# Kernel tuning notes

Hardware: AMD Instinct MI355X
Metric: run time of the kernel (lower is better)

Reference implementation:

```python
import jax, jax.numpy as jnp
import numpy as np

N_HEADS = 16
D_HEAD = 64
D_MODEL = 1024


def apply_rotary_emb(t, cos, sin):
    # t: (B, H, T, D), cos/sin: (T, D//2) -> half-split rotation
    d2 = t.shape[-1] // 2
    t1, t2 = t[..., :d2], t[..., d2:]
    cos = cos[None, None, :, :]
    sin = sin[None, None, :, :]
    return jnp.concatenate([t1 * cos - t2 * sin, t1 * sin + t2 * cos], axis=-1)


def setup_inputs() -> dict:
    key = jax.random.key(0)
    ks = jax.random.split(key, 8)
    B, T = 2, 2048
    x = jax.random.normal(ks[0], (B, T, D_MODEL), dtype=jnp.float32)
    # rotary cache built from standard inv-freq schedule
    inv_freq = 1.0 / (10000.0 ** (jnp.arange(0, D_HEAD, 2, dtype=jnp.float32) / D_HEAD))
    ang = jnp.arange(T, dtype=jnp.float32)[:, None] * inv_freq[None, :]  # (T, D/2)
    cos, sin = jnp.cos(ang), jnp.sin(ang)
    s = 1.0 / np.sqrt(D_MODEL)
    W_q = jax.random.normal(ks[1], (D_MODEL, N_HEADS * D_HEAD), dtype=jnp.float32) * s
    W_k = jax.random.normal(ks[2], (D_MODEL, N_HEADS * D_HEAD), dtype=jnp.float32) * s
    W_v = jax.random.normal(ks[3], (D_MODEL, N_HEADS * D_HEAD), dtype=jnp.float32) * s
    W_out = jax.random.normal(ks[4], (N_HEADS * D_HEAD, D_MODEL), dtype=jnp.float32) * s
    return {"x": x, "cos": cos, "sin": sin, "W_q": W_q, "W_k": W_k, "W_v": W_v, "W_out": W_out}


def reference(x, cos, sin, W_q, W_k, W_v, W_out):
    B, T, _ = x.shape
    def split_heads(t):
        return t.reshape(B, T, N_HEADS, D_HEAD).transpose(0, 2, 1, 3)  # (B,H,T,D)
    q = split_heads(x @ W_q)
    k = split_heads(x @ W_k)
    v = split_heads(x @ W_v)
    q = apply_rotary_emb(q, cos, sin)
    k = apply_rotary_emb(k, cos, sin)
    scores = jnp.einsum('bhqd,bhkd->bhqk', q, k) / np.sqrt(D_HEAD).astype(np.float32)
    causal = jnp.triu(jnp.ones((T, T), dtype=bool), k=1)
    scores = jnp.where(causal[None, None], -jnp.inf, scores)
    attn = jax.nn.softmax(scores, axis=-1)
    z = jnp.einsum('bhqk,bhkd->bhqd', attn, v)
    z = z.transpose(0, 2, 1, 3).reshape(B, T, N_HEADS * D_HEAD)
    return z @ W_out
```

## Files before the change

### kernel.cpp

```cpp
#include <hip/hip_runtime.h>

typedef __attribute__((ext_vector_type(4))) float f32x4;
typedef __attribute__((ext_vector_type(8))) short short8;
typedef __attribute__((ext_vector_type(8))) unsigned short u16x8;
typedef __attribute__((ext_vector_type(4))) unsigned short u16x4;
typedef __attribute__((ext_vector_type(2))) unsigned int u32x2;

#define D_MODEL 1024
#define NHEADS 16
#define T_SEQ 2048
#define M_TOT 4096

__device__ __forceinline__ unsigned short f2bf(float f) {
    union { float f; unsigned int u; } v; v.f = f;
    return (unsigned short)((v.u + 0x7fffu + ((v.u >> 16) & 1u)) >> 16);
}
__device__ __forceinline__ float bf2f(unsigned short b) {
    union { unsigned int u; float f; } v; v.u = ((unsigned int)b) << 16;
    return v.f;
}
__device__ __forceinline__ unsigned int cvtpk_bf16(float lo, float hi) {
    unsigned int r;
    asm("v_cvt_pk_bf16_f32 %0, %1, %2" : "=v"(r) : "v"(lo), "v"(hi));
    return r;
}

#define GLD0(dst, addr) \
    asm volatile("global_load_dwordx4 %0, %1, off" : "=v"(dst) : "v"(addr) : "memory")
#define WAITV0() do { asm volatile("s_waitcnt vmcnt(0)" ::: "memory"); \
                      __builtin_amdgcn_sched_barrier(0); } while (0)
#define LBAR() do { asm volatile("s_waitcnt lgkmcnt(0)" ::: "memory"); \
                    __builtin_amdgcn_s_barrier(); \
                    __builtin_amdgcn_sched_barrier(0); } while (0)

__global__ __launch_bounds__(256) void convert_x_kernel(const float* __restrict__ X,
                                                        unsigned short* __restrict__ Xb) {
    const int i = (blockIdx.x * 256 + threadIdx.x) * 4;
    const float4 v = *(const float4*)(X + i);
    u16x4 r;
    r.x = f2bf(v.x); r.y = f2bf(v.y); r.z = f2bf(v.z); r.w = f2bf(v.w);
    *(u16x4*)(Xb + i) = r;
}

__global__ __launch_bounds__(256) void transpose_w_kernel(const float* __restrict__ W0,
                                                          const float* __restrict__ W1,
                                                          const float* __restrict__ W2,
                                                          const float* __restrict__ W3,
                                                          unsigned short* __restrict__ Wt0) {
    __shared__ float tile[64][65];
    const int z = blockIdx.z;
    const float* W = (z == 0) ? W0 : (z == 1) ? W1 : (z == 2) ? W2 : W3;
    unsigned short* Wt = Wt0 + (size_t)z * D_MODEL * D_MODEL;
    const int n0 = blockIdx.x * 64, k0 = blockIdx.y * 64;
    for (int i = threadIdx.x; i < 4096; i += 256) {
        const int r = i >> 6, c = i & 63;
        tile[r][c] = W[(size_t)(k0 + r) * D_MODEL + n0 + c];
    }
    __syncthreads();
    for (int i = threadIdx.x; i < 4096; i += 256) {
        const int r = i >> 6, c = i & 63;
        Wt[(size_t)(n0 + r) * D_MODEL + k0 + c] = f2bf(tile[c][r]);
    }
}

#define TN_G 128
#define BK_G 32
#define BKP_G 36

template<int MI, int OUTMODE>
__global__ __launch_bounds__(256) void gemm_kernel(
    const unsigned short* __restrict__ A,
    const unsigned short* __restrict__ Bt0,
    void* __restrict__ Cout0,
    const float* __restrict__ cosp,
    const float* __restrict__ sinp)
{
    constexpr int TMc = MI * 32;
    constexpr int NA = (TMc * 4) / 256;
    __shared__ unsigned short sA[TMc * BKP_G];
    __shared__ unsigned short sB[TN_G * BKP_G];

    const int tid = threadIdx.x;
    const int wid = tid >> 6;
    const int lane = tid & 63;
    const int quad = lane >> 4;
    const int l16 = lane & 15;
    const int wm = wid >> 1, wn = wid & 1;
    const int m0 = blockIdx.x * TMc, n0 = blockIdx.y * TN_G;
    const int z = blockIdx.z;
    const unsigned short* Bt = Bt0 + (size_t)z * D_MODEL * D_MODEL;

    f32x4 acc[MI][4] = {};

    for (int k0 = 0; k0 < D_MODEL; k0 += BK_G) {
        u16x8 av[NA], bv[2];
        #pragma unroll
        for (int i = 0; i < NA; ++i) {
            const int c = tid + i * 256, r = c >> 2, sg = (c & 3) * 8;
            av[i] = *(const u16x8*)(A + (size_t)(m0 + r) * D_MODEL + k0 + sg);
        }
        #pragma unroll
        for (int i = 0; i < 2; ++i) {
            const int c = tid + i * 256, r = c >> 2, sg = (c & 3) * 8;
            bv[i] = *(const u16x8*)(Bt + (size_t)(n0 + r) * D_MODEL + k0 + sg);
        }
        __syncthreads();
        #pragma unroll
        for (int i = 0; i < NA; ++i) {
            const int c = tid + i * 256, r = c >> 2, sg = (c & 3) * 8;
            *(u16x8*)&sA[r * BKP_G + sg] = av[i];
        }
        #pragma unroll
        for (int i = 0; i < 2; ++i) {
            const int c = tid + i * 256, r = c >> 2, sg = (c & 3) * 8;
            *(u16x8*)&sB[r * BKP_G + sg] = bv[i];
        }
        __syncthreads();

        short8 af[MI], bf[4];
        #pragma unroll
        for (int i = 0; i < MI; ++i)
            af[i] = *(const short8*)&sA[(wm * (MI * 16) + i * 16 + l16) * BKP_G + quad * 8];
        #pragma unroll
        for (int i = 0; i < 4; ++i)
            bf[i] = *(const short8*)&sB[(wn * 64 + i * 16 + l16) * BKP_G + quad * 8];
        #pragma unroll
        for (int mi = 0; mi < MI; ++mi)
            #pragma unroll
            for (int ni = 0; ni < 4; ++ni)
                acc[mi][ni] = __builtin_amdgcn_mfma_f32_16x16x32_bf16(af[mi], bf[ni], acc[mi][ni], 0, 0, 0);
    }

    if constexpr (OUTMODE == 0) {
        float* C = (float*)Cout0;
        #pragma unroll
        for (int mi = 0; mi < MI; ++mi) {
            const int mb = m0 + wm * (MI * 16) + mi * 16 + quad * 4;
            #pragma unroll
            for (int ni = 0; ni < 4; ++ni) {
                const int n = n0 + wn * 64 + ni * 16 + l16;
                #pragma unroll
                for (int r = 0; r < 4; ++r)
                    C[(size_t)(mb + r) * D_MODEL + n] = acc[mi][ni][r];
            }
        }
    } else {
        unsigned short* O = (unsigned short*)Cout0 + (size_t)z * M_TOT * D_MODEL;
        const int h = (n0 + wn * 64) >> 6;
        if (z == 2) {
            #pragma unroll
            for (int mi = 0; mi < MI; ++mi) {
                const int mb = m0 + wm * (MI * 16) + mi * 16 + quad * 4;
                const int b = mb >> 11, t = mb & (T_SEQ - 1);
                #pragma unroll
                for (int ni = 0; ni < 4; ++ni) {
                    const int d = ni * 16 + l16;
                    u16x4 pk;
                    #pragma unroll
                    for (int r = 0; r < 4; ++r) pk[r] = f2bf(acc[mi][ni][r]);
                    *(u16x4*)(O + ((size_t)(b * NHEADS + h) * 64 + d) * T_SEQ + t) = pk;
                }
            }
        } else {
            const float qs = (z == 0) ? 0.125f : 1.0f;
            #pragma unroll
            for (int mi = 0; mi < MI; ++mi) {
                #pragma unroll
                for (int r = 0; r < 4; ++r) {
                    const int m = m0 + wm * (MI * 16) + mi * 16 + quad * 4 + r;
                    const int b = m >> 11, t = m & (T_SEQ - 1);
                    const size_t rowoff = ((size_t)(b * NHEADS + h) * T_SEQ + t) * 64;
                    #pragma unroll
                    for (int ni = 0; ni < 2; ++ni) {
                        const int d = ni * 16 + l16;
                        const float c = cosp[t * 32 + d], s = sinp[t * 32 + d];
                        const float x1 = acc[mi][ni][r], x2 = acc[mi][ni + 2][r];
                        O[rowoff + d]      = f2bf((x1 * c - x2 * s) * qs);
                        O[rowoff + d + 32] = f2bf((x1 * s + x2 * c) * qs);
                    }
                }
            }
        }
    }
}

__global__ __launch_bounds__(256) void kmax_kernel(const unsigned short* __restrict__ Kg,
                                                   float* __restrict__ Kseg) {
    __shared__ float red[4];
    const int seg = blockIdx.x, bh = blockIdx.y;
    const unsigned short* Kp = Kg + ((size_t)bh * T_SEQ + seg * 256) * 64;
    const int row = threadIdx.x;
    const u16x8* rp = (const u16x8*)(Kp + (size_t)row * 64);
    float s = 0.f;
    #pragma unroll
    for (int c = 0; c < 8; ++c) {
        const u16x8 v = rp[c];
        #pragma unroll
        for (int e = 0; e < 8; ++e) { const float f = bf2f(v[e]); s += f * f; }
    }
    #pragma unroll
    for (int off = 32; off >= 1; off >>= 1) s = fmaxf(s, __shfl_xor(s, off));
    if ((threadIdx.x & 63) == 0) red[threadIdx.x >> 6] = s;
    __syncthreads();
    if (threadIdx.x == 0)
        Kseg[bh * 8 + seg] = __builtin_sqrtf(fmaxf(fmaxf(red[0], red[1]), fmaxf(red[2], red[3])));
}

#define LOG2E 1.44269504f

struct AttnSmem {
    union {
        unsigned short kv[2][4][4096];
        float comb[4][64][34];
    } u;
    unsigned short P[8][16 * 64];
};

__global__ __launch_bounds__(512, 2) void attn_kernel(
    const unsigned short* __restrict__ Q,
    const unsigned short* __restrict__ Kg,
    const unsigned short* __restrict__ Vt,
    const float* __restrict__ Kseg,
    unsigned short* __restrict__ Z)
{
    __shared__ AttnSmem sm;

    const int tid = threadIdx.x;
    const int wid = tid >> 6;
    const int w4 = wid & 3;
    const int half = wid >> 2;
    const int lane = tid & 63;
    const int quad = lane >> 4;
    const int l16 = lane & 15;
    const int srow = tid >> 3;
    const int sslot = tid & 7;
    const int wslot = sslot ^ (srow & 7);
    const int sxK = (quad ^ (l16 & 7)) << 3;
    const int ph8 = (l16 & 7) << 3;

    const int flat = blockIdx.x + 16 * blockIdx.y;
    const int xcd = flat & 7, idx = flat >> 3;
    const int bh = xcd * 4 + (idx & 3);
    const int x = idx >> 2;

    const int qA = x, qB = 31 - x;
    const int jend = 31 - x;

    const unsigned short* Qp = Q + (size_t)bh * T_SEQ * 64;
    const unsigned short* Kp = Kg + (size_t)bh * T_SEQ * 64;
    const unsigned short* Vp = Vt + (size_t)bh * 64 * T_SEQ;

    short8 aqA[2], aqB[2];
    {
        const unsigned short* qr = Qp + (size_t)(qA * 64 + w4 * 16 + l16) * 64 + quad * 8;
        aqA[0] = *(const short8*)(qr);
        aqA[1] = *(const short8*)(qr + 32);
        qr = Qp + (size_t)(qB * 64 + w4 * 16 + l16) * 64 + quad * 8;
        aqB[0] = *(const short8*)(qr);
        aqB[1] = *(const short8*)(qr + 32);
    }

    float kmx = 0.f;
    #pragma unroll
    for (int i = 0; i < 8; ++i) kmx = fmaxf(kmx, Kseg[bh * 8 + i]);

    float mQA, mQB;
    {
        float nqA = 0.f, nqB = 0.f;
        #pragma unroll
        for (int i = 0; i < 2; ++i)
            #pragma unroll
            for (int e = 0; e < 8; ++e) {
                const float fa = bf2f((unsigned short)aqA[i][e]);
                const float fb = bf2f((unsigned short)aqB[i][e]);
                nqA += fa * fa; nqB += fb * fb;
            }
        nqA += __shfl_xor(nqA, 16); nqA += __shfl_xor(nqA, 32);
        nqB += __shfl_xor(nqB, 16); nqB += __shfl_xor(nqB, 32);
        mQA = __builtin_sqrtf(nqA) * kmx * LOG2E;
        mQB = __builtin_sqrtf(nqB) * kmx * LOG2E;
    }

    auto tile_pack = [&](f32x4 (&s)[4], float mQ, float& lsum, bool msk,
                         unsigned short* Pw) {
        if (msk) {
            #pragma unroll
            for (int nt = 0; nt < 4; ++nt)
                #pragma unroll
                for (int r = 0; r < 4; ++r)
                    if (nt * 16 + quad * 4 + r > w4 * 16 + l16) s[nt][r] = -1e30f;
        }
        #pragma unroll
        for (int nt = 0; nt < 4; ++nt) {
            const float p0 = __builtin_exp2f(s[nt][0] * LOG2E - mQ);
            const float p1 = __builtin_exp2f(s[nt][1] * LOG2E - mQ);
            const float p2 = __builtin_exp2f(s[nt][2] * LOG2E - mQ);
            const float p3 = __builtin_exp2f(s[nt][3] * LOG2E - mQ);
            lsum += (p0 + p1) + (p2 + p3);
            const unsigned int w0 = cvtpk_bf16(p0, p1);
            const unsigned int w1 = cvtpk_bf16(p2, p3);
            *(u32x2*)&Pw[l16 * 64 + ((nt * 16 + quad * 4) ^ ph8)] = (u32x2){w0, w1};
        }
    };

    f32x4 oA[4] = {}, oB[4] = {};
    float lA = 0.f, lB = 0.f;
    unsigned short* Pw = &sm.P[wid][0];

    short8 stg[4];
    auto ISSUE = [&](int t) {
        const int j0 = 2 * t, j1 = j0 + 1;
        GLD0(stg[0], Kp + (size_t)j0 * 4096 + tid * 8);
        GLD0(stg[1], Vp + (size_t)srow * 2048 + j0 * 64 + sslot * 8);
        GLD0(stg[2], Kp + (size_t)j1 * 4096 + tid * 8);
        GLD0(stg[3], Vp + (size_t)srow * 2048 + j1 * 64 + sslot * 8);
    };
    auto WRITE = [&](int b) {
        const int dst = srow * 64 + (wslot << 3);
        *(short8*)&sm.u.kv[b][0][dst] = stg[0];
        *(short8*)&sm.u.kv[b][1][dst] = stg[1];
        *(short8*)&sm.u.kv[b][2][dst] = stg[2];
        *(short8*)&sm.u.kv[b][3][dst] = stg[3];
    };

    auto COMPUTE = [&](int j, int b) {
        if (j > jend) return;
        const bool doA = (j <= x);
        const unsigned short* sKb = &sm.u.kv[b][half * 2][0];
        const unsigned short* sVb = &sm.u.kv[b][half * 2 + 1][0];
        f32x4 sA[4] = {}, sB[4] = {};
        __builtin_amdgcn_s_setprio(1);
        #pragma unroll
        for (int nt = 0; nt < 4; ++nt) {
            const int rb = (nt * 16 + l16) * 64;
            const short8 k0 = *(const short8*)&sKb[rb + sxK];
            const short8 k1 = *(const short8*)&sKb[rb + (sxK ^ 32)];
            if (doA) {
                sA[nt] = __builtin_amdgcn_mfma_f32_16x16x32_bf16(k0, aqA[0], sA[nt], 0, 0, 0);
                sA[nt] = __builtin_amdgcn_mfma_f32_16x16x32_bf16(k1, aqA[1], sA[nt], 0, 0, 0);
            }
            sB[nt] = __builtin_amdgcn_mfma_f32_16x16x32_bf16(k0, aqB[0], sB[nt], 0, 0, 0);
            sB[nt] = __builtin_amdgcn_mfma_f32_16x16x32_bf16(k1, aqB[1], sB[nt], 0, 0, 0);
        }
        __builtin_amdgcn_s_setprio(0);
        short8 pfA0 = {}, pfA1 = {};
        if (doA) {
            tile_pack(sA, mQA, lA, j == x, Pw);
            asm volatile("s_waitcnt lgkmcnt(0)" ::: "memory");
            pfA0 = *(const short8*)&Pw[l16 * 64 + ((quad * 8) ^ ph8)];
            pfA1 = *(const short8*)&Pw[l16 * 64 + ((32 + quad * 8) ^ ph8)];
        }
        tile_pack(sB, mQB, lB, j == jend, Pw);
        asm volatile("s_waitcnt lgkmcnt(0)" ::: "memory");
        const short8 pfB0 = *(const short8*)&Pw[l16 * 64 + ((quad * 8) ^ ph8)];
        const short8 pfB1 = *(const short8*)&Pw[l16 * 64 + ((32 + quad * 8) ^ ph8)];
        __builtin_amdgcn_s_setprio(1);
        #pragma unroll
        for (int dt = 0; dt < 4; ++dt) {
            const int rb = (dt * 16 + l16) * 64;
            const short8 v0 = *(const short8*)&sVb[rb + sxK];
            const short8 v1 = *(const short8*)&sVb[rb + (sxK ^ 32)];
            if (doA) {
                oA[dt] = __builtin_amdgcn_mfma_f32_16x16x32_bf16(pfA0, v0, oA[dt], 0, 0, 0);
                oA[dt] = __builtin_amdgcn_mfma_f32_16x16x32_bf16(pfA1, v1, oA[dt], 0, 0, 0);
            }
            oB[dt] = __builtin_amdgcn_mfma_f32_16x16x32_bf16(pfB0, v0, oB[dt], 0, 0, 0);
            oB[dt] = __builtin_amdgcn_mfma_f32_16x16x32_bf16(pfB1, v1, oB[dt], 0, 0, 0);
        }
        __builtin_amdgcn_s_setprio(0);
    };

    const int nr = (jend >> 1) + 1;
    ISSUE(0);
    WAITV0();
    WRITE(0);
    LBAR();
    for (int t = 0; t < nr; ++t) {
        const bool more = (t + 1 < nr);
        if (more) ISSUE(t + 1);
        COMPUTE(2 * t + half, t & 1);
        if (more) {
            WAITV0();
            WRITE((t + 1) & 1);
        }
        LBAR();
    }

    lA += __shfl_xor(lA, 16); lA += __shfl_xor(lA, 32);
    lB += __shfl_xor(lB, 16); lB += __shfl_xor(lB, 32);

    __syncthreads();
    if (half) {
        float* cb = &sm.u.comb[w4][lane][0];
        #pragma unroll
        for (int dt = 0; dt < 4; ++dt)
            #pragma unroll
            for (int r = 0; r < 4; ++r) {
                cb[dt * 4 + r]      = oA[dt][r];
                cb[16 + dt * 4 + r] = oB[dt][r];
            }
        cb[32] = lA; cb[33] = lB;
    }
    __syncthreads();
    if (half) return;

    {
        const float* cb = &sm.u.comb[w4][lane][0];
        #pragma unroll
        for (int dt = 0; dt < 4; ++dt)
            #pragma unroll
            for (int r = 0; r < 4; ++r) {
                oA[dt][r] += cb[dt * 4 + r];
                oB[dt][r] += cb[16 + dt * 4 + r];
            }
        lA += cb[32]; lB += cb[33];
    }

    const float iA = 1.f / lA, iB = 1.f / lB;
    float irA[4], irB[4];
    #pragma unroll
    for (int r = 0; r < 4; ++r) {
        const int src = (lane & 48) | (quad * 4 + r);
        irA[r] = __shfl(iA, src);
        irB[r] = __shfl(iB, src);
    }

    const int h = bh & 15, b = bh >> 4;
    #pragma unroll
    for (int dt = 0; dt < 4; ++dt)
        #pragma unroll
        for (int r = 0; r < 4; ++r) {
            const int rowA = qA * 64 + w4 * 16 + quad * 4 + r;
            const int rowB = qB * 64 + w4 * 16 + quad * 4 + r;
            const int col = h * 64 + dt * 16 + l16;
            Z[((size_t)b * T_SEQ + rowA) * D_MODEL + col] = f2bf(oA[dt][r] * irA[r]);
            Z[((size_t)b * T_SEQ + rowB) * D_MODEL + col] = f2bf(oB[dt][r] * irB[r]);
        }
}

extern "C" void kernel_launch(void* const* d_in, const int* in_sizes, int n_in,
                              void* d_out, int out_size, void* d_ws, size_t ws_size,
                              hipStream_t stream) {
    const float* x    = (const float*)d_in[0];
    const float* cosp = (const float*)d_in[1];
    const float* sinp = (const float*)d_in[2];
    const float* Wq   = (const float*)d_in[3];
    const float* Wk   = (const float*)d_in[4];
    const float* Wv   = (const float*)d_in[5];
    const float* Wo   = (const float*)d_in[6];

    char* w = (char*)d_ws;
    unsigned short* xb  = (unsigned short*)w; w += (size_t)M_TOT * D_MODEL * 2;
    unsigned short* wt  = (unsigned short*)w; w += (size_t)4 * D_MODEL * D_MODEL * 2;
    unsigned short* Qb  = (unsigned short*)w; w += (size_t)M_TOT * D_MODEL * 2;
    unsigned short* Kb  = (unsigned short*)w; w += (size_t)M_TOT * D_MODEL * 2;
    unsigned short* Vtb = (unsigned short*)w; w += (size_t)M_TOT * D_MODEL * 2;
    unsigned short* Zb  = (unsigned short*)w; w += (size_t)M_TOT * D_MODEL * 2;
    float*          Ks  = (float*)w;          w += 32 * 8 * sizeof(float);

    convert_x_kernel<<<(M_TOT * D_MODEL) / 1024, 256, 0, stream>>>(x, xb);
    transpose_w_kernel<<<dim3(16, 16, 4), 256, 0, stream>>>(Wq, Wk, Wv, Wo, wt);

    gemm_kernel<4, 1><<<dim3(M_TOT / 128, D_MODEL / 128, 3), 256, 0, stream>>>(
        xb, wt, (void*)Qb, cosp, sinp);

    kmax_kernel<<<dim3(8, 32), 256, 0, stream>>>(Kb, Ks);

    attn_kernel<<<dim3(16, 32), 512, 0, stream>>>(Qb, Kb, Vtb, Ks, Zb);

    gemm_kernel<2, 0><<<dim3(M_TOT / 64, D_MODEL / 128, 1), 256, 0, stream>>>(
        Zb, wt + (size_t)3 * D_MODEL * D_MODEL, d_out, nullptr, nullptr);
}
```

Measured before the change: 216.1 us.

## Fuse prep kernels, fold K-norm max into projection GEMM, use direct-to-LDS loads

Merges the x conversion and weight transpose into one launch. Computes per-64-row K norm maxima in the QKV GEMM epilogue, which removes the separate kmax pass that re-read K. The GEMM mainloop now uses global_load_lds to move tiles straight into unpadded shared memory, dropping the register staging and one barrier per k-step. Without padding, LDS fragment reads may see more bank conflicts, and there is still no double buffering.

```diff
diff --git a/kernel.cpp b/kernel.cpp
--- a/kernel.cpp
+++ b/kernel.cpp
@@ -33,22 +33,28 @@
                     __builtin_amdgcn_s_barrier(); \
                     __builtin_amdgcn_sched_barrier(0); } while (0)
 
-__global__ __launch_bounds__(256) void convert_x_kernel(const float* __restrict__ X,
-                                                        unsigned short* __restrict__ Xb) {
-    const int i = (blockIdx.x * 256 + threadIdx.x) * 4;
-    const float4 v = *(const float4*)(X + i);
-    u16x4 r;
-    r.x = f2bf(v.x); r.y = f2bf(v.y); r.z = f2bf(v.z); r.w = f2bf(v.w);
-    *(u16x4*)(Xb + i) = r;
-}
-
-__global__ __launch_bounds__(256) void transpose_w_kernel(const float* __restrict__ W0,
-                                                          const float* __restrict__ W1,
-                                                          const float* __restrict__ W2,
-                                                          const float* __restrict__ W3,
-                                                          unsigned short* __restrict__ Wt0) {
+#define GLDS16(gp, lp) \
+    __builtin_amdgcn_global_load_lds((const __attribute__((address_space(1))) void*)(gp), \
+                                     (__attribute__((address_space(3))) void*)(lp), 16, 0, 0)
+
+__global__ __launch_bounds__(256) void prep_kernel(const float* __restrict__ X,
+                                                   unsigned short* __restrict__ Xb,
+                                                   const float* __restrict__ W0,
+                                                   const float* __restrict__ W1,
+                                                   const float* __restrict__ W2,
+                                                   const float* __restrict__ W3,
+                                                   unsigned short* __restrict__ Wt0) {
     __shared__ float tile[64][65];
     const int z = blockIdx.z;
+    if (z >= 4) {
+        const int blk = (z - 4) * 256 + blockIdx.y * 16 + blockIdx.x;
+        const int i = (blk * 256 + threadIdx.x) * 4;
+        const float4 v = *(const float4*)(X + i);
+        u16x4 r;
+        r.x = f2bf(v.x); r.y = f2bf(v.y); r.z = f2bf(v.z); r.w = f2bf(v.w);
+        *(u16x4*)(Xb + i) = r;
+        return;
+    }
     const float* W = (z == 0) ? W0 : (z == 1) ? W1 : (z == 2) ? W2 : W3;
     unsigned short* Wt = Wt0 + (size_t)z * D_MODEL * D_MODEL;
     const int n0 = blockIdx.x * 64, k0 = blockIdx.y * 64;
@@ -65,7 +71,6 @@
 
 #define TN_G 128
 #define BK_G 32
-#define BKP_G 36
 
 template<int MI, int OUTMODE>
 __global__ __launch_bounds__(256) void gemm_kernel(
@@ -73,12 +78,13 @@
     const unsigned short* __restrict__ Bt0,
     void* __restrict__ Cout0,
     const float* __restrict__ cosp,
-    const float* __restrict__ sinp)
+    const float* __restrict__ sinp,
+    float* __restrict__ Kmax)
 {
     constexpr int TMc = MI * 32;
-    constexpr int NA = (TMc * 4) / 256;
-    __shared__ unsigned short sA[TMc * BKP_G];
-    __shared__ unsigned short sB[TN_G * BKP_G];
+    constexpr int NCHA = TMc / 16;
+    __shared__ unsigned short sA[TMc * 32];
+    __shared__ unsigned short sB[TN_G * 32];
 
     const int tid = threadIdx.x;
     const int wid = tid >> 6;
@@ -89,46 +95,37 @@
     const int m0 = blockIdx.x * TMc, n0 = blockIdx.y * TN_G;
     const int z = blockIdx.z;
     const unsigned short* Bt = Bt0 + (size_t)z * D_MODEL * D_MODEL;
+    const int srowL = lane >> 2;
+    const int scolL = (lane & 3) * 8;
 
     f32x4 acc[MI][4] = {};
 
     for (int k0 = 0; k0 < D_MODEL; k0 += BK_G) {
-        u16x8 av[NA], bv[2];
-        #pragma unroll
-        for (int i = 0; i < NA; ++i) {
-            const int c = tid + i * 256, r = c >> 2, sg = (c & 3) * 8;
-            av[i] = *(const u16x8*)(A + (size_t)(m0 + r) * D_MODEL + k0 + sg);
-        }
-        #pragma unroll
-        for (int i = 0; i < 2; ++i) {
-            const int c = tid + i * 256, r = c >> 2, sg = (c & 3) * 8;
-            bv[i] = *(const u16x8*)(Bt + (size_t)(n0 + r) * D_MODEL + k0 + sg);
+        #pragma unroll
+        for (int ch = wid; ch < NCHA + 8; ch += 4) {
+            if (ch < NCHA) {
+                GLDS16(A + (size_t)(m0 + ch * 16 + srowL) * D_MODEL + k0 + scolL,
+                       &sA[ch * 512]);
+            } else {
+                GLDS16(Bt + (size_t)(n0 + (ch - NCHA) * 16 + srowL) * D_MODEL + k0 + scolL,
+                       &sB[(ch - NCHA) * 512]);
+            }
         }
         __syncthreads();
-        #pragma unroll
-        for (int i = 0; i < NA; ++i) {
-            const int c = tid + i * 256, r = c >> 2, sg = (c & 3) * 8;
-            *(u16x8*)&sA[r * BKP_G + sg] = av[i];
-        }
-        #pragma unroll
-        for (int i = 0; i < 2; ++i) {
-            const int c = tid + i * 256, r = c >> 2, sg = (c & 3) * 8;
-            *(u16x8*)&sB[r * BKP_G + sg] = bv[i];
-        }
-        __syncthreads();
 
         short8 af[MI], bf[4];
         #pragma unroll
         for (int i = 0; i < MI; ++i)
-            af[i] = *(const short8*)&sA[(wm * (MI * 16) + i * 16 + l16) * BKP_G + quad * 8];
+            af[i] = *(const short8*)&sA[(wm * (MI * 16) + i * 16 + l16) * 32 + quad * 8];
         #pragma unroll
         for (int i = 0; i < 4; ++i)
-            bf[i] = *(const short8*)&sB[(wn * 64 + i * 16 + l16) * BKP_G + quad * 8];
+            bf[i] = *(const short8*)&sB[(wn * 64 + i * 16 + l16) * 32 + quad * 8];
         #pragma unroll
         for (int mi = 0; mi < MI; ++mi)
             #pragma unroll
             for (int ni = 0; ni < 4; ++ni)
                 acc[mi][ni] = __builtin_amdgcn_mfma_f32_16x16x32_bf16(af[mi], bf[ni], acc[mi][ni], 0, 0, 0);
+        __syncthreads();
     }
 
     if constexpr (OUTMODE == 0) {
@@ -162,6 +159,27 @@
                 }
             }
         } else {
+            if (z == 1) {
+                float mx = 0.f;
+                #pragma unroll
+                for (int mi = 0; mi < MI; ++mi)
+                    #pragma unroll
+                    for (int r = 0; r < 4; ++r) {
+                        float s = 0.f;
+                        #pragma unroll
+                        for (int ni = 0; ni < 4; ++ni) s += acc[mi][ni][r] * acc[mi][ni][r];
+                        s += __shfl_xor(s, 1); s += __shfl_xor(s, 2);
+                        s += __shfl_xor(s, 4); s += __shfl_xor(s, 8);
+                        mx = fmaxf(mx, s);
+                    }
+                mx = fmaxf(mx, __shfl_xor(mx, 16));
+                mx = fmaxf(mx, __shfl_xor(mx, 32));
+                if (lane == 0) {
+                    const int b = m0 >> 11;
+                    const int slot = ((m0 >> 7) & 15) * 2 + wm;
+                    Kmax[(size_t)(b * NHEADS + h) * 32 + slot] = __builtin_sqrtf(mx);
+                }
+            }
             const float qs = (z == 0) ? 0.125f : 1.0f;
             #pragma unroll
             for (int mi = 0; mi < MI; ++mi) {
@@ -184,28 +202,6 @@
     }
 }
 
-__global__ __launch_bounds__(256) void kmax_kernel(const unsigned short* __restrict__ Kg,
-                                                   float* __restrict__ Kseg) {
-    __shared__ float red[4];
-    const int seg = blockIdx.x, bh = blockIdx.y;
-    const unsigned short* Kp = Kg + ((size_t)bh * T_SEQ + seg * 256) * 64;
-    const int row = threadIdx.x;
-    const u16x8* rp = (const u16x8*)(Kp + (size_t)row * 64);
-    float s = 0.f;
-    #pragma unroll
-    for (int c = 0; c < 8; ++c) {
-        const u16x8 v = rp[c];
-        #pragma unroll
-        for (int e = 0; e < 8; ++e) { const float f = bf2f(v[e]); s += f * f; }
-    }
-    #pragma unroll
-    for (int off = 32; off >= 1; off >>= 1) s = fmaxf(s, __shfl_xor(s, off));
-    if ((threadIdx.x & 63) == 0) red[threadIdx.x >> 6] = s;
-    __syncthreads();
-    if (threadIdx.x == 0)
-        Kseg[bh * 8 + seg] = __builtin_sqrtf(fmaxf(fmaxf(red[0], red[1]), fmaxf(red[2], red[3])));
-}
-
 #define LOG2E 1.44269504f
 
 struct AttnSmem {
@@ -262,7 +258,7 @@
 
     float kmx = 0.f;
     #pragma unroll
-    for (int i = 0; i < 8; ++i) kmx = fmaxf(kmx, Kseg[bh * 8 + i]);
+    for (int i = 0; i < 32; ++i) kmx = fmaxf(kmx, Kseg[bh * 32 + i]);
 
     float mQA, mQB;
     {
@@ -456,18 +452,15 @@
     unsigned short* Kb  = (unsigned short*)w; w += (size_t)M_TOT * D_MODEL * 2;
     unsigned short* Vtb = (unsigned short*)w; w += (size_t)M_TOT * D_MODEL * 2;
     unsigned short* Zb  = (unsigned short*)w; w += (size_t)M_TOT * D_MODEL * 2;
-    float*          Ks  = (float*)w;          w += 32 * 8 * sizeof(float);
-
-    convert_x_kernel<<<(M_TOT * D_MODEL) / 1024, 256, 0, stream>>>(x, xb);
-    transpose_w_kernel<<<dim3(16, 16, 4), 256, 0, stream>>>(Wq, Wk, Wv, Wo, wt);
+    float*          Ks  = (float*)w;          w += 32 * 32 * sizeof(float);
+
+    prep_kernel<<<dim3(16, 16, 20), 256, 0, stream>>>(x, xb, Wq, Wk, Wv, Wo, wt);
 
     gemm_kernel<4, 1><<<dim3(M_TOT / 128, D_MODEL / 128, 3), 256, 0, stream>>>(
-        xb, wt, (void*)Qb, cosp, sinp);
-
-    kmax_kernel<<<dim3(8, 32), 256, 0, stream>>>(Kb, Ks);
+        xb, wt, (void*)Qb, cosp, sinp, Ks);
 
     attn_kernel<<<dim3(16, 32), 512, 0, stream>>>(Qb, Kb, Vtb, Ks, Zb);
 
     gemm_kernel<2, 0><<<dim3(M_TOT / 64, D_MODEL / 128, 1), 256, 0, stream>>>(
-        Zb, wt + (size_t)3 * D_MODEL * D_MODEL, d_out, nullptr, nullptr);
-}
+        Zb, wt + (size_t)3 * D_MODEL * D_MODEL, d_out, nullptr, nullptr, nullptr);
+}
```

Measured after the change: 212.2 us. About the same (-1.8%).
